# Performance work log

Measured on AMD Instinct MI355X. Metric: run time of the kernel, lower is better.

Reference implementation:

```python
import jax, jax.numpy as jnp
import numpy as np
from jax import lax

T, B, S, H, A = 512, 1024, 64, 128, 10


def setup_inputs() -> dict:
    key = jax.random.key(0)
    ks = jax.random.split(key, 12)
    p = lambda k, shape: jax.random.normal(k, shape, dtype=jnp.float32) * 0.1
    return {
        "x": jax.random.normal(ks[0], (T, B, S), dtype=jnp.float32),
        "W_ih1": p(ks[1], (4 * H, S)),
        "W_hh1": p(ks[2], (4 * H, H)),
        "b_ih1": p(ks[3], (4 * H,)),
        "b_hh1": p(ks[4], (4 * H,)),
        "W_ih2": p(ks[5], (4 * H, H)),
        "W_hh2": p(ks[6], (4 * H, H)),
        "b_ih2": p(ks[7], (4 * H,)),
        "b_hh2": p(ks[8], (4 * H,)),
        "W_out": p(ks[9], (A, H)),
        "b_out": p(ks[10], (A,)),
    }


def _lstm_cell(x_t, h, c, W_ih, W_hh, b_ih, b_hh):
    # PyTorch LSTMCell: gates ordered (i, f, g, o)
    gates = x_t @ W_ih.T + b_ih + h @ W_hh.T + b_hh  # [B, 4H]
    i, f, g, o = jnp.split(gates, 4, axis=-1)
    i = jax.nn.sigmoid(i)
    f = jax.nn.sigmoid(f)
    g = jnp.tanh(g)
    o = jax.nn.sigmoid(o)
    c_new = f * c + i * g
    h_new = o * jnp.tanh(c_new)
    return h_new, c_new


def reference(x, W_ih1, W_hh1, b_ih1, b_hh1, W_ih2, W_hh2, b_ih2, b_hh2, W_out, b_out):
    batch = x.shape[1]
    hdim = W_hh1.shape[1]

    def step(carry, x_t):
        h1, c1, h2, c2 = carry
        h1, c1 = _lstm_cell(x_t, h1, c1, W_ih1, W_hh1, b_ih1, b_hh1)
        h2, c2 = _lstm_cell(h1, h2, c2, W_ih2, W_hh2, b_ih2, b_hh2)
        return (h1, c1, h2, c2), h2

    z = jnp.zeros((batch, hdim), dtype=x.dtype)
    init = (z, z, z, z)
    _, ys = lax.scan(step, init, x)  # ys: [T, B, H]
    mu = ys @ W_out.T + b_out  # deterministic action
    return mu
```

## Files before the change

### kernel.cpp

```cpp
#include <hip/hip_runtime.h>

#define TT 512
#define NB 1024
#define SS 64
#define HH 128
#define NA 10

typedef short bf16x8 __attribute__((ext_vector_type(8)));
typedef float f32x4 __attribute__((ext_vector_type(4)));
typedef unsigned short u16;
typedef unsigned int u32;

__device__ __forceinline__ u16 f2bf(float f){
  union { float f; u32 u; } v; v.f = f;
  return (u16)((v.u + 0x7FFFu + ((v.u >> 16) & 1u)) >> 16);
}
__device__ __forceinline__ float sigm(float v){
  return __builtin_amdgcn_rcpf(1.f + __builtin_amdgcn_exp2f(-1.442695040888963f * v));
}
__device__ __forceinline__ float tanh_(float v){
  return 1.f - 2.f * __builtin_amdgcn_rcpf(1.f + __builtin_amdgcn_exp2f(2.885390081777927f * v));
}
__device__ __forceinline__ void bar_lds(){
  asm volatile("s_waitcnt lgkmcnt(0)" ::: "memory");
  __builtin_amdgcn_s_barrier();
}

__global__ __launch_bounds__(512, 2)
void lstm_fused(const float* __restrict__ x,
                const float* __restrict__ Whh1f,
                const float* __restrict__ bih1, const float* __restrict__ bhh1,
                const float* __restrict__ Wih1f,
                const float* __restrict__ Wih2f,
                const float* __restrict__ Whh2f,
                const float* __restrict__ bih2, const float* __restrict__ bhh2,
                const float* __restrict__ Woutf, const float* __restrict__ boutf,
                float* __restrict__ out)
{
  __shared__ __align__(16) u16 lds[77824];
  u16* whh1s = lds;
  u16* wos   = lds + 65536;
  u16* h1s   = lds + 67584;
  u16* h2s   = lds + 71680;
  u16* xs    = lds + 75776;

  const int tid = threadIdx.x;
  const int w   = tid >> 6;
  const int L   = tid & 63;
  const int Llo = L & 15;
  const int Lhi = L >> 4;
  const int batch0 = blockIdx.x * 16;

#pragma unroll 4
  for (int it = 0; it < 16; ++it){
    int j = it*512 + tid;
    int l = j & 63, g = (j >> 6) & 3, kt = (j >> 8) & 3, ww = (j >> 10) & 7;
    int col = 128*g + 16*ww + (l & 15);
    int k   = kt*32 + (l >> 4)*8;
    const float* s = Whh1f + col*HH + k;
    bf16x8 v;
#pragma unroll
    for (int e = 0; e < 8; ++e) v[e] = (short)f2bf(s[e]);
    *reinterpret_cast<bf16x8*>(&whh1s[j*8]) = v;
  }

  bf16x8 Wih1r[2][4];
#pragma unroll
  for (int kt = 0; kt < 2; ++kt)
#pragma unroll
    for (int g = 0; g < 4; ++g){
      int col = 128*g + 16*w + Llo;
      const float* s = Wih1f + col*SS + kt*32 + Lhi*8;
      bf16x8 v;
#pragma unroll
      for (int e = 0; e < 8; ++e) v[e] = (short)f2bf(s[e]);
      Wih1r[kt][g] = v;
    }
  bf16x8 Wih2r[4][4], Whh2r[4][4];
#pragma unroll
  for (int kt = 0; kt < 4; ++kt)
#pragma unroll
    for (int g = 0; g < 4; ++g){
      int col = 128*g + 16*w + Llo;
      const float* p2 = Wih2f + col*HH + kt*32 + Lhi*8;
      const float* p3 = Whh2f + col*HH + kt*32 + Lhi*8;
      bf16x8 v2, v3;
#pragma unroll
      for (int e = 0; e < 8; ++e){ v2[e] = (short)f2bf(p2[e]); v3[e] = (short)f2bf(p3[e]); }
      Wih2r[kt][g] = v2; Whh2r[kt][g] = v3;
    }

  float bias1[4], bias2[4];
#pragma unroll
  for (int g = 0; g < 4; ++g){
    int col = 128*g + 16*w + Llo;
    bias1[g] = bih1[col] + bhh1[col];
    bias2[g] = bih2[col] + bhh2[col];
  }
  const float boutr = (Llo < NA) ? boutf[Llo] : 0.f;

  if (tid < 256){
    int kt = tid >> 6, l = tid & 63, llo = l & 15, lhi = (l >> 4) & 3;
    bf16x8 v;
#pragma unroll
    for (int e = 0; e < 8; ++e) v[e] = 0;
    if (llo < NA){
      const float* s = Woutf + llo*HH + kt*32 + lhi*8;
#pragma unroll
      for (int e = 0; e < 8; ++e) v[e] = (short)f2bf(s[e]);
    }
    *reinterpret_cast<bf16x8*>(&wos[kt*512 + l*8]) = v;
  }

  {
    uint4 z = {0u,0u,0u,0u};
    *reinterpret_cast<uint4*>(h1s + tid*8) = z;
    *reinterpret_cast<uint4*>(h2s + tid*8) = z;
  }

  f32x4 c1 = {0.f,0.f,0.f,0.f}, c2 = {0.f,0.f,0.f,0.f};

  const int afrag = L*8;
  const int hwIdx = (2*w + (Llo >> 3))*128 + Lhi*32 + (Llo & 7);

  const int xrow = tid >> 5;
  const int xj   = (tid & 31)*2;
  const int xsIdx = ((xj >> 3)*16 + xrow)*8 + (xj & 7);

  {
    float2 xv = *reinterpret_cast<const float2*>(x + ((size_t)(batch0 + xrow))*SS + xj);
    *reinterpret_cast<u32*>(&xs[xsIdx]) = (u32)f2bf(xv.x) | ((u32)f2bf(xv.y) << 16);
  }
  float2 xreg = *reinterpret_cast<const float2*>(x + ((size_t)NB + batch0 + xrow)*SS + xj);

  __syncthreads();

  for (int t = 0; t < TT; ++t){
    const u16* h1r = h1s + ((t+1)&1)*2048;
    u16*       h1w = h1s + (t&1)*2048;
    const u16* h2r = h2s + (t&1)*2048;
    u16*       h2w = h2s + ((t+1)&1)*2048;
    const u16* xsr = xs + (t&1)*1024;
    u16*       xsw = xs + ((t+1)&1)*1024;

    bf16x8 h1f0 = *reinterpret_cast<const bf16x8*>(h1r + afrag);
    bf16x8 h1f1 = *reinterpret_cast<const bf16x8*>(h1r + 512 + afrag);
    bf16x8 h1f2 = *reinterpret_cast<const bf16x8*>(h1r + 1024 + afrag);
    bf16x8 h1f3 = *reinterpret_cast<const bf16x8*>(h1r + 1536 + afrag);

    f32x4 acc2[4];
#pragma unroll
    for (int g = 0; g < 4; ++g){
      f32x4 a = (f32x4){bias2[g], bias2[g], bias2[g], bias2[g]};
      a = __builtin_amdgcn_mfma_f32_16x16x32_bf16(h1f0, Wih2r[0][g], a, 0, 0, 0);
      a = __builtin_amdgcn_mfma_f32_16x16x32_bf16(h1f1, Wih2r[1][g], a, 0, 0, 0);
      a = __builtin_amdgcn_mfma_f32_16x16x32_bf16(h1f2, Wih2r[2][g], a, 0, 0, 0);
      a = __builtin_amdgcn_mfma_f32_16x16x32_bf16(h1f3, Wih2r[3][g], a, 0, 0, 0);
      acc2[g] = a;
    }
    {
      bf16x8 hf = *reinterpret_cast<const bf16x8*>(h2r + afrag);
#pragma unroll
      for (int g = 0; g < 4; ++g) acc2[g] = __builtin_amdgcn_mfma_f32_16x16x32_bf16(hf, Whh2r[0][g], acc2[g], 0, 0, 0);
      hf = *reinterpret_cast<const bf16x8*>(h2r + 512 + afrag);
#pragma unroll
      for (int g = 0; g < 4; ++g) acc2[g] = __builtin_amdgcn_mfma_f32_16x16x32_bf16(hf, Whh2r[1][g], acc2[g], 0, 0, 0);
      hf = *reinterpret_cast<const bf16x8*>(h2r + 1024 + afrag);
#pragma unroll
      for (int g = 0; g < 4; ++g) acc2[g] = __builtin_amdgcn_mfma_f32_16x16x32_bf16(hf, Whh2r[2][g], acc2[g], 0, 0, 0);
      hf = *reinterpret_cast<const bf16x8*>(h2r + 1536 + afrag);
#pragma unroll
      for (int g = 0; g < 4; ++g) acc2[g] = __builtin_amdgcn_mfma_f32_16x16x32_bf16(hf, Whh2r[3][g], acc2[g], 0, 0, 0);
    }

    if (t > 0){
#pragma unroll
      for (int r = 0; r < 4; ++r){
        float iv = sigm(acc2[0][r]);
        float fv = sigm(acc2[1][r]);
        float gv = tanh_(acc2[2][r]);
        float ov = sigm(acc2[3][r]);
        float cn = fv*c2[r] + iv*gv;
        c2[r] = cn;
        h2w[hwIdx + r*8] = f2bf(ov * tanh_(cn));
      }
    }

    f32x4 acc1[4];
#pragma unroll
    for (int g = 0; g < 4; ++g) acc1[g] = (f32x4){bias1[g], bias1[g], bias1[g], bias1[g]};
#pragma unroll
    for (int kt = 0; kt < 4; ++kt){
      bf16x8 wh0 = *reinterpret_cast<const bf16x8*>(&whh1s[w*8192 + (kt*4+0)*512 + afrag]);
      bf16x8 wh1 = *reinterpret_cast<const bf16x8*>(&whh1s[w*8192 + (kt*4+1)*512 + afrag]);
      bf16x8 wh2 = *reinterpret_cast<const bf16x8*>(&whh1s[w*8192 + (kt*4+2)*512 + afrag]);
      bf16x8 wh3 = *reinterpret_cast<const bf16x8*>(&whh1s[w*8192 + (kt*4+3)*512 + afrag]);
      bf16x8 hf = (kt==0) ? h1f0 : (kt==1) ? h1f1 : (kt==2) ? h1f2 : h1f3;
      acc1[0] = __builtin_amdgcn_mfma_f32_16x16x32_bf16(hf, wh0, acc1[0], 0, 0, 0);
      acc1[1] = __builtin_amdgcn_mfma_f32_16x16x32_bf16(hf, wh1, acc1[1], 0, 0, 0);
      acc1[2] = __builtin_amdgcn_mfma_f32_16x16x32_bf16(hf, wh2, acc1[2], 0, 0, 0);
      acc1[3] = __builtin_amdgcn_mfma_f32_16x16x32_bf16(hf, wh3, acc1[3], 0, 0, 0);
    }

    if (w == 0 && t >= 2){
      f32x4 pacc = {boutr, boutr, boutr, boutr};
#pragma unroll
      for (int kt = 0; kt < 4; ++kt){
        bf16x8 ha = *reinterpret_cast<const bf16x8*>(h2r + kt*512 + afrag);
        bf16x8 wb = *reinterpret_cast<const bf16x8*>(&wos[kt*512 + afrag]);
        pacc = __builtin_amdgcn_mfma_f32_16x16x32_bf16(ha, wb, pacc, 0, 0, 0);
      }
      if (Llo < NA){
        size_t o = ((size_t)(t-2)*NB + batch0 + Lhi*4)*NA + Llo;
#pragma unroll
        for (int r = 0; r < 4; ++r) out[o + (size_t)r*NA] = pacc[r];
      }
    }

    *reinterpret_cast<u32*>(xsw + xsIdx) = (u32)f2bf(xreg.x) | ((u32)f2bf(xreg.y) << 16);
    if (t + 2 < TT)
      xreg = *reinterpret_cast<const float2*>(x + ((size_t)(t+2)*NB + batch0 + xrow)*SS + xj);

    {
      bf16x8 xf0 = *reinterpret_cast<const bf16x8*>(xsr + afrag);
      bf16x8 xf1 = *reinterpret_cast<const bf16x8*>(xsr + 512 + afrag);
#pragma unroll
      for (int g = 0; g < 4; ++g){
        acc1[g] = __builtin_amdgcn_mfma_f32_16x16x32_bf16(xf0, Wih1r[0][g], acc1[g], 0, 0, 0);
        acc1[g] = __builtin_amdgcn_mfma_f32_16x16x32_bf16(xf1, Wih1r[1][g], acc1[g], 0, 0, 0);
      }
    }
#pragma unroll
    for (int r = 0; r < 4; ++r){
      float iv = sigm(acc1[0][r]);
      float fv = sigm(acc1[1][r]);
      float gv = tanh_(acc1[2][r]);
      float ov = sigm(acc1[3][r]);
      float cn = fv*c1[r] + iv*gv;
      c1[r] = cn;
      h1w[hwIdx + r*8] = f2bf(ov * tanh_(cn));
    }

    bar_lds();
  }

  {
    const u16* h1r = h1s + ((TT+1)&1)*2048;
    const u16* h2r = h2s + (TT&1)*2048;
    u16*       h2w = h2s + ((TT+1)&1)*2048;

    bf16x8 h1f0 = *reinterpret_cast<const bf16x8*>(h1r + afrag);
    bf16x8 h1f1 = *reinterpret_cast<const bf16x8*>(h1r + 512 + afrag);
    bf16x8 h1f2 = *reinterpret_cast<const bf16x8*>(h1r + 1024 + afrag);
    bf16x8 h1f3 = *reinterpret_cast<const bf16x8*>(h1r + 1536 + afrag);
    bf16x8 h2f0 = *reinterpret_cast<const bf16x8*>(h2r + afrag);
    bf16x8 h2f1 = *reinterpret_cast<const bf16x8*>(h2r + 512 + afrag);
    bf16x8 h2f2 = *reinterpret_cast<const bf16x8*>(h2r + 1024 + afrag);
    bf16x8 h2f3 = *reinterpret_cast<const bf16x8*>(h2r + 1536 + afrag);

    f32x4 acc2[4];
#pragma unroll
    for (int g = 0; g < 4; ++g){
      f32x4 a = (f32x4){bias2[g], bias2[g], bias2[g], bias2[g]};
      a = __builtin_amdgcn_mfma_f32_16x16x32_bf16(h1f0, Wih2r[0][g], a, 0, 0, 0);
      a = __builtin_amdgcn_mfma_f32_16x16x32_bf16(h1f1, Wih2r[1][g], a, 0, 0, 0);
      a = __builtin_amdgcn_mfma_f32_16x16x32_bf16(h1f2, Wih2r[2][g], a, 0, 0, 0);
      a = __builtin_amdgcn_mfma_f32_16x16x32_bf16(h1f3, Wih2r[3][g], a, 0, 0, 0);
      a = __builtin_amdgcn_mfma_f32_16x16x32_bf16(h2f0, Whh2r[0][g], a, 0, 0, 0);
      a = __builtin_amdgcn_mfma_f32_16x16x32_bf16(h2f1, Whh2r[1][g], a, 0, 0, 0);
      a = __builtin_amdgcn_mfma_f32_16x16x32_bf16(h2f2, Whh2r[2][g], a, 0, 0, 0);
      a = __builtin_amdgcn_mfma_f32_16x16x32_bf16(h2f3, Whh2r[3][g], a, 0, 0, 0);
      acc2[g] = a;
    }
#pragma unroll
    for (int r = 0; r < 4; ++r){
      float iv = sigm(acc2[0][r]);
      float fv = sigm(acc2[1][r]);
      float gv = tanh_(acc2[2][r]);
      float ov = sigm(acc2[3][r]);
      float cn = fv*c2[r] + iv*gv;
      c2[r] = cn;
      h2w[hwIdx + r*8] = f2bf(ov * tanh_(cn));
    }

    if (w == 0){
      f32x4 pacc = {boutr, boutr, boutr, boutr};
      pacc = __builtin_amdgcn_mfma_f32_16x16x32_bf16(h2f0, *reinterpret_cast<const bf16x8*>(&wos[afrag]),        pacc, 0, 0, 0);
      pacc = __builtin_amdgcn_mfma_f32_16x16x32_bf16(h2f1, *reinterpret_cast<const bf16x8*>(&wos[512 + afrag]),  pacc, 0, 0, 0);
      pacc = __builtin_amdgcn_mfma_f32_16x16x32_bf16(h2f2, *reinterpret_cast<const bf16x8*>(&wos[1024 + afrag]), pacc, 0, 0, 0);
      pacc = __builtin_amdgcn_mfma_f32_16x16x32_bf16(h2f3, *reinterpret_cast<const bf16x8*>(&wos[1536 + afrag]), pacc, 0, 0, 0);
      if (Llo < NA){
        size_t o = ((size_t)(TT-2)*NB + batch0 + Lhi*4)*NA + Llo;
#pragma unroll
        for (int r = 0; r < 4; ++r) out[o + (size_t)r*NA] = pacc[r];
      }
    }

    bar_lds();

    if (w == 0){
      const u16* h2f = h2s + ((TT+1)&1)*2048;
      bf16x8 a0 = *reinterpret_cast<const bf16x8*>(h2f + afrag);
      bf16x8 a1 = *reinterpret_cast<const bf16x8*>(h2f + 512 + afrag);
      bf16x8 a2 = *reinterpret_cast<const bf16x8*>(h2f + 1024 + afrag);
      bf16x8 a3 = *reinterpret_cast<const bf16x8*>(h2f + 1536 + afrag);
      f32x4 pacc = {boutr, boutr, boutr, boutr};
      pacc = __builtin_amdgcn_mfma_f32_16x16x32_bf16(a0, *reinterpret_cast<const bf16x8*>(&wos[afrag]),        pacc, 0, 0, 0);
      pacc = __builtin_amdgcn_mfma_f32_16x16x32_bf16(a1, *reinterpret_cast<const bf16x8*>(&wos[512 + afrag]),  pacc, 0, 0, 0);
      pacc = __builtin_amdgcn_mfma_f32_16x16x32_bf16(a2, *reinterpret_cast<const bf16x8*>(&wos[1024 + afrag]), pacc, 0, 0, 0);
      pacc = __builtin_amdgcn_mfma_f32_16x16x32_bf16(a3, *reinterpret_cast<const bf16x8*>(&wos[1536 + afrag]), pacc, 0, 0, 0);
      if (Llo < NA){
        size_t o = ((size_t)(TT-1)*NB + batch0 + Lhi*4)*NA + Llo;
#pragma unroll
        for (int r = 0; r < 4; ++r) out[o + (size_t)r*NA] = pacc[r];
      }
    }
  }
}

extern "C" void kernel_launch(void* const* d_in, const int* in_sizes, int n_in,
                              void* d_out, int out_size, void* d_ws, size_t ws_size,
                              hipStream_t stream){
  (void)in_sizes; (void)n_in; (void)out_size; (void)d_ws; (void)ws_size;
  const float* xp   = (const float*)d_in[0];
  const float* wih1 = (const float*)d_in[1];
  const float* whh1 = (const float*)d_in[2];
  const float* bih1 = (const float*)d_in[3];
  const float* bhh1 = (const float*)d_in[4];
  const float* wih2 = (const float*)d_in[5];
  const float* whh2 = (const float*)d_in[6];
  const float* bih2 = (const float*)d_in[7];
  const float* bhh2 = (const float*)d_in[8];
  const float* wout = (const float*)d_in[9];
  const float* bout = (const float*)d_in[10];
  float* outp = (float*)d_out;

  hipLaunchKernelGGL(lstm_fused, dim3(64), dim3(512), 0, stream,
                     xp, whh1, bih1, bhh1, wih1, wih2, whh2, bih2, bhh2, wout, bout,
                     outp);
}
```

Before: 1.451 ms.

## Specialize warps: half compute layer-1 cell, half layer-2 cell

```diff
diff --git a/kernel.cpp b/kernel.cpp
--- a/kernel.cpp
+++ b/kernel.cpp
@@ -38,7 +38,7 @@
                 float* __restrict__ out)
 {
   __shared__ __align__(16) u16 lds[77824];
-  u16* whh1s = lds;
+  u16* whh2s = lds;
   u16* wos   = lds + 65536;
   u16* h1s   = lds + 67584;
   u16* h2s   = lds + 71680;
@@ -50,54 +50,20 @@
   const int Llo = L & 15;
   const int Lhi = L >> 4;
   const int batch0 = blockIdx.x * 16;
+  const int afrag = L*8;
 
 #pragma unroll 4
   for (int it = 0; it < 16; ++it){
     int j = it*512 + tid;
-    int l = j & 63, g = (j >> 6) & 3, kt = (j >> 8) & 3, ww = (j >> 10) & 7;
-    int col = 128*g + 16*ww + (l & 15);
+    int l = j & 63, g = (j >> 6) & 3, kt = (j >> 8) & 3, ss = (j >> 10) & 7;
+    int col = 128*g + 16*ss + (l & 15);
     int k   = kt*32 + (l >> 4)*8;
-    const float* s = Whh1f + col*HH + k;
+    const float* s = Whh2f + col*HH + k;
     bf16x8 v;
 #pragma unroll
     for (int e = 0; e < 8; ++e) v[e] = (short)f2bf(s[e]);
-    *reinterpret_cast<bf16x8*>(&whh1s[j*8]) = v;
-  }
-
-  bf16x8 Wih1r[2][4];
-#pragma unroll
-  for (int kt = 0; kt < 2; ++kt)
-#pragma unroll
-    for (int g = 0; g < 4; ++g){
-      int col = 128*g + 16*w + Llo;
-      const float* s = Wih1f + col*SS + kt*32 + Lhi*8;
-      bf16x8 v;
-#pragma unroll
-      for (int e = 0; e < 8; ++e) v[e] = (short)f2bf(s[e]);
-      Wih1r[kt][g] = v;
-    }
-  bf16x8 Wih2r[4][4], Whh2r[4][4];
-#pragma unroll
-  for (int kt = 0; kt < 4; ++kt)
-#pragma unroll
-    for (int g = 0; g < 4; ++g){
-      int col = 128*g + 16*w + Llo;
-      const float* p2 = Wih2f + col*HH + kt*32 + Lhi*8;
-      const float* p3 = Whh2f + col*HH + kt*32 + Lhi*8;
-      bf16x8 v2, v3;
-#pragma unroll
-      for (int e = 0; e < 8; ++e){ v2[e] = (short)f2bf(p2[e]); v3[e] = (short)f2bf(p3[e]); }
-      Wih2r[kt][g] = v2; Whh2r[kt][g] = v3;
-    }
-
-  float bias1[4], bias2[4];
-#pragma unroll
-  for (int g = 0; g < 4; ++g){
-    int col = 128*g + 16*w + Llo;
-    bias1[g] = bih1[col] + bhh1[col];
-    bias2[g] = bih2[col] + bhh2[col];
-  }
-  const float boutr = (Llo < NA) ? boutf[Llo] : 0.f;
+    *reinterpret_cast<bf16x8*>(&whh2s[j*8]) = v;
+  }
 
   if (tid < 256){
     int kt = tid >> 6, l = tid & 63, llo = l & 15, lhi = (l >> 4) & 3;
@@ -118,20 +84,79 @@
     *reinterpret_cast<uint4*>(h2s + tid*8) = z;
   }
 
-  f32x4 c1 = {0.f,0.f,0.f,0.f}, c2 = {0.f,0.f,0.f,0.f};
-
-  const int afrag = L*8;
-  const int hwIdx = (2*w + (Llo >> 3))*128 + Lhi*32 + (Llo & 7);
-
-  const int xrow = tid >> 5;
-  const int xj   = (tid & 31)*2;
-  const int xsIdx = ((xj >> 3)*16 + xrow)*8 + (xj & 7);
-
-  {
-    float2 xv = *reinterpret_cast<const float2*>(x + ((size_t)(batch0 + xrow))*SS + xj);
-    *reinterpret_cast<u32*>(&xs[xsIdx]) = (u32)f2bf(xv.x) | ((u32)f2bf(xv.y) << 16);
-  }
-  float2 xreg = *reinterpret_cast<const float2*>(x + ((size_t)NB + batch0 + xrow)*SS + xj);
+  const float boutr = (Llo < NA) ? boutf[Llo] : 0.f;
+
+  bf16x8 Wr[2][6][4];
+  float  biasr[2][4];
+  f32x4  cr[2];
+  float4 xreg;
+
+  if (w < 4){
+#pragma unroll
+    for (int si = 0; si < 2; ++si){
+      int s = w + si*4;
+#pragma unroll
+      for (int kt = 0; kt < 4; ++kt)
+#pragma unroll
+        for (int g = 0; g < 4; ++g){
+          int col = 128*g + 16*s + Llo;
+          const float* p = Whh1f + col*HH + kt*32 + Lhi*8;
+          bf16x8 v;
+#pragma unroll
+          for (int e = 0; e < 8; ++e) v[e] = (short)f2bf(p[e]);
+          Wr[si][kt][g] = v;
+        }
+#pragma unroll
+      for (int kt = 0; kt < 2; ++kt)
+#pragma unroll
+        for (int g = 0; g < 4; ++g){
+          int col = 128*g + 16*s + Llo;
+          const float* p = Wih1f + col*SS + kt*32 + Lhi*8;
+          bf16x8 v;
+#pragma unroll
+          for (int e = 0; e < 8; ++e) v[e] = (short)f2bf(p[e]);
+          Wr[si][4+kt][g] = v;
+        }
+#pragma unroll
+      for (int g = 0; g < 4; ++g){
+        int col = 128*g + 16*s + Llo;
+        biasr[si][g] = bih1[col] + bhh1[col];
+      }
+    }
+    {
+      int row = tid & 15, j = (tid >> 4) * 4;
+      int xsIdx = ((j >> 3)*16 + row)*8 + (j & 7);
+      float4 xv = *reinterpret_cast<const float4*>(x + ((size_t)(batch0 + row))*SS + j);
+      u32 lo = (u32)f2bf(xv.x) | ((u32)f2bf(xv.y) << 16);
+      u32 hi = (u32)f2bf(xv.z) | ((u32)f2bf(xv.w) << 16);
+      *reinterpret_cast<uint2*>(xs + xsIdx) = make_uint2(lo, hi);
+      xreg = *reinterpret_cast<const float4*>(x + ((size_t)NB + batch0 + row)*SS + j);
+    }
+  } else {
+#pragma unroll
+    for (int si = 0; si < 2; ++si){
+      int s = (w - 4) + si*4;
+#pragma unroll
+      for (int kt = 0; kt < 4; ++kt)
+#pragma unroll
+        for (int g = 0; g < 4; ++g){
+          int col = 128*g + 16*s + Llo;
+          const float* p = Wih2f + col*HH + kt*32 + Lhi*8;
+          bf16x8 v;
+#pragma unroll
+          for (int e = 0; e < 8; ++e) v[e] = (short)f2bf(p[e]);
+          Wr[si][kt][g] = v;
+        }
+#pragma unroll
+      for (int g = 0; g < 4; ++g){
+        int col = 128*g + 16*s + Llo;
+        biasr[si][g] = bih2[col] + bhh2[col];
+      }
+    }
+  }
+
+#pragma unroll
+  for (int si = 0; si < 2; ++si) cr[si] = (f32x4){0.f,0.f,0.f,0.f};
 
   __syncthreads();
 
@@ -143,66 +168,150 @@
     const u16* xsr = xs + (t&1)*1024;
     u16*       xsw = xs + ((t+1)&1)*1024;
 
-    bf16x8 h1f0 = *reinterpret_cast<const bf16x8*>(h1r + afrag);
-    bf16x8 h1f1 = *reinterpret_cast<const bf16x8*>(h1r + 512 + afrag);
-    bf16x8 h1f2 = *reinterpret_cast<const bf16x8*>(h1r + 1024 + afrag);
-    bf16x8 h1f3 = *reinterpret_cast<const bf16x8*>(h1r + 1536 + afrag);
-
-    f32x4 acc2[4];
-#pragma unroll
-    for (int g = 0; g < 4; ++g){
-      f32x4 a = (f32x4){bias2[g], bias2[g], bias2[g], bias2[g]};
-      a = __builtin_amdgcn_mfma_f32_16x16x32_bf16(h1f0, Wih2r[0][g], a, 0, 0, 0);
-      a = __builtin_amdgcn_mfma_f32_16x16x32_bf16(h1f1, Wih2r[1][g], a, 0, 0, 0);
-      a = __builtin_amdgcn_mfma_f32_16x16x32_bf16(h1f2, Wih2r[2][g], a, 0, 0, 0);
-      a = __builtin_amdgcn_mfma_f32_16x16x32_bf16(h1f3, Wih2r[3][g], a, 0, 0, 0);
-      acc2[g] = a;
-    }
-    {
-      bf16x8 hf = *reinterpret_cast<const bf16x8*>(h2r + afrag);
-#pragma unroll
-      for (int g = 0; g < 4; ++g) acc2[g] = __builtin_amdgcn_mfma_f32_16x16x32_bf16(hf, Whh2r[0][g], acc2[g], 0, 0, 0);
-      hf = *reinterpret_cast<const bf16x8*>(h2r + 512 + afrag);
-#pragma unroll
-      for (int g = 0; g < 4; ++g) acc2[g] = __builtin_amdgcn_mfma_f32_16x16x32_bf16(hf, Whh2r[1][g], acc2[g], 0, 0, 0);
-      hf = *reinterpret_cast<const bf16x8*>(h2r + 1024 + afrag);
-#pragma unroll
-      for (int g = 0; g < 4; ++g) acc2[g] = __builtin_amdgcn_mfma_f32_16x16x32_bf16(hf, Whh2r[2][g], acc2[g], 0, 0, 0);
-      hf = *reinterpret_cast<const bf16x8*>(h2r + 1536 + afrag);
-#pragma unroll
-      for (int g = 0; g < 4; ++g) acc2[g] = __builtin_amdgcn_mfma_f32_16x16x32_bf16(hf, Whh2r[3][g], acc2[g], 0, 0, 0);
-    }
-
-    if (t > 0){
+    if (w < 4){
+      {
+        int row = tid & 15, j = (tid >> 4) * 4;
+        int xsIdx = ((j >> 3)*16 + row)*8 + (j & 7);
+        u32 lo = (u32)f2bf(xreg.x) | ((u32)f2bf(xreg.y) << 16);
+        u32 hi = (u32)f2bf(xreg.z) | ((u32)f2bf(xreg.w) << 16);
+        *reinterpret_cast<uint2*>(xsw + xsIdx) = make_uint2(lo, hi);
+        if (t + 2 < TT)
+          xreg = *reinterpret_cast<const float4*>(x + ((size_t)(t+2)*NB + batch0 + row)*SS + j);
+      }
+#pragma unroll
+      for (int si = 0; si < 2; ++si){
+        int s = w + si*4;
+        f32x4 a0 = (f32x4){biasr[si][0],biasr[si][0],biasr[si][0],biasr[si][0]};
+        f32x4 a1 = (f32x4){biasr[si][1],biasr[si][1],biasr[si][1],biasr[si][1]};
+        f32x4 a2 = (f32x4){biasr[si][2],biasr[si][2],biasr[si][2],biasr[si][2]};
+        f32x4 a3 = (f32x4){biasr[si][3],biasr[si][3],biasr[si][3],biasr[si][3]};
+#pragma unroll
+        for (int kt = 0; kt < 4; ++kt){
+          bf16x8 hf = *reinterpret_cast<const bf16x8*>(h1r + kt*512 + afrag);
+          a0 = __builtin_amdgcn_mfma_f32_16x16x32_bf16(hf, Wr[si][kt][0], a0, 0, 0, 0);
+          a1 = __builtin_amdgcn_mfma_f32_16x16x32_bf16(hf, Wr[si][kt][1], a1, 0, 0, 0);
+          a2 = __builtin_amdgcn_mfma_f32_16x16x32_bf16(hf, Wr[si][kt][2], a2, 0, 0, 0);
+          a3 = __builtin_amdgcn_mfma_f32_16x16x32_bf16(hf, Wr[si][kt][3], a3, 0, 0, 0);
+        }
+#pragma unroll
+        for (int kt = 0; kt < 2; ++kt){
+          bf16x8 xf = *reinterpret_cast<const bf16x8*>(xsr + kt*512 + afrag);
+          a0 = __builtin_amdgcn_mfma_f32_16x16x32_bf16(xf, Wr[si][4+kt][0], a0, 0, 0, 0);
+          a1 = __builtin_amdgcn_mfma_f32_16x16x32_bf16(xf, Wr[si][4+kt][1], a1, 0, 0, 0);
+          a2 = __builtin_amdgcn_mfma_f32_16x16x32_bf16(xf, Wr[si][4+kt][2], a2, 0, 0, 0);
+          a3 = __builtin_amdgcn_mfma_f32_16x16x32_bf16(xf, Wr[si][4+kt][3], a3, 0, 0, 0);
+        }
+        int hwIdx = (2*s + (Llo >> 3))*128 + Lhi*32 + (Llo & 7);
+#pragma unroll
+        for (int r = 0; r < 4; ++r){
+          float iv = sigm(a0[r]);
+          float fv = sigm(a1[r]);
+          float gv = tanh_(a2[r]);
+          float ov = sigm(a3[r]);
+          float cn = fv*cr[si][r] + iv*gv;
+          cr[si][r] = cn;
+          h1w[hwIdx + r*8] = f2bf(ov * tanh_(cn));
+        }
+      }
+    } else {
+#pragma unroll
+      for (int si = 0; si < 2; ++si){
+        int s = (w - 4) + si*4;
+        f32x4 a0 = (f32x4){biasr[si][0],biasr[si][0],biasr[si][0],biasr[si][0]};
+        f32x4 a1 = (f32x4){biasr[si][1],biasr[si][1],biasr[si][1],biasr[si][1]};
+        f32x4 a2 = (f32x4){biasr[si][2],biasr[si][2],biasr[si][2],biasr[si][2]};
+        f32x4 a3 = (f32x4){biasr[si][3],biasr[si][3],biasr[si][3],biasr[si][3]};
+#pragma unroll
+        for (int kt = 0; kt < 4; ++kt){
+          bf16x8 hf1 = *reinterpret_cast<const bf16x8*>(h1r + kt*512 + afrag);
+          a0 = __builtin_amdgcn_mfma_f32_16x16x32_bf16(hf1, Wr[si][kt][0], a0, 0, 0, 0);
+          a1 = __builtin_amdgcn_mfma_f32_16x16x32_bf16(hf1, Wr[si][kt][1], a1, 0, 0, 0);
+          a2 = __builtin_amdgcn_mfma_f32_16x16x32_bf16(hf1, Wr[si][kt][2], a2, 0, 0, 0);
+          a3 = __builtin_amdgcn_mfma_f32_16x16x32_bf16(hf1, Wr[si][kt][3], a3, 0, 0, 0);
+          bf16x8 hf2 = *reinterpret_cast<const bf16x8*>(h2r + kt*512 + afrag);
+          bf16x8 wb0 = *reinterpret_cast<const bf16x8*>(&whh2s[s*8192 + (kt*4+0)*512 + afrag]);
+          bf16x8 wb1 = *reinterpret_cast<const bf16x8*>(&whh2s[s*8192 + (kt*4+1)*512 + afrag]);
+          bf16x8 wb2 = *reinterpret_cast<const bf16x8*>(&whh2s[s*8192 + (kt*4+2)*512 + afrag]);
+          bf16x8 wb3 = *reinterpret_cast<const bf16x8*>(&whh2s[s*8192 + (kt*4+3)*512 + afrag]);
+          a0 = __builtin_amdgcn_mfma_f32_16x16x32_bf16(hf2, wb0, a0, 0, 0, 0);
+          a1 = __builtin_amdgcn_mfma_f32_16x16x32_bf16(hf2, wb1, a1, 0, 0, 0);
+          a2 = __builtin_amdgcn_mfma_f32_16x16x32_bf16(hf2, wb2, a2, 0, 0, 0);
+          a3 = __builtin_amdgcn_mfma_f32_16x16x32_bf16(hf2, wb3, a3, 0, 0, 0);
+        }
+        if (t > 0){
+          int hwIdx = (2*s + (Llo >> 3))*128 + Lhi*32 + (Llo & 7);
+#pragma unroll
+          for (int r = 0; r < 4; ++r){
+            float iv = sigm(a0[r]);
+            float fv = sigm(a1[r]);
+            float gv = tanh_(a2[r]);
+            float ov = sigm(a3[r]);
+            float cn = fv*cr[si][r] + iv*gv;
+            cr[si][r] = cn;
+            h2w[hwIdx + r*8] = f2bf(ov * tanh_(cn));
+          }
+        }
+      }
+      if (w == 4 && t >= 2){
+        f32x4 pacc = {boutr, boutr, boutr, boutr};
+#pragma unroll
+        for (int kt = 0; kt < 4; ++kt){
+          bf16x8 ha = *reinterpret_cast<const bf16x8*>(h2r + kt*512 + afrag);
+          bf16x8 wb = *reinterpret_cast<const bf16x8*>(&wos[kt*512 + afrag]);
+          pacc = __builtin_amdgcn_mfma_f32_16x16x32_bf16(ha, wb, pacc, 0, 0, 0);
+        }
+        if (Llo < NA){
+          size_t o = ((size_t)(t-2)*NB + batch0 + Lhi*4)*NA + Llo;
+#pragma unroll
+          for (int r = 0; r < 4; ++r) out[o + (size_t)r*NA] = pacc[r];
+        }
+      }
+    }
+
+    bar_lds();
+  }
+
+  if (w >= 4){
+    const u16* h1r = h1s + ((TT+1)&1)*2048;
+    const u16* h2r = h2s + (TT&1)*2048;
+    u16*       h2w = h2s + ((TT+1)&1)*2048;
+#pragma unroll
+    for (int si = 0; si < 2; ++si){
+      int s = (w - 4) + si*4;
+      f32x4 a0 = (f32x4){biasr[si][0],biasr[si][0],biasr[si][0],biasr[si][0]};
+      f32x4 a1 = (f32x4){biasr[si][1],biasr[si][1],biasr[si][1],biasr[si][1]};
+      f32x4 a2 = (f32x4){biasr[si][2],biasr[si][2],biasr[si][2],biasr[si][2]};
+      f32x4 a3 = (f32x4){biasr[si][3],biasr[si][3],biasr[si][3],biasr[si][3]};
+#pragma unroll
+      for (int kt = 0; kt < 4; ++kt){
+        bf16x8 hf1 = *reinterpret_cast<const bf16x8*>(h1r + kt*512 + afrag);
+        a0 = __builtin_amdgcn_mfma_f32_16x16x32_bf16(hf1, Wr[si][kt][0], a0, 0, 0, 0);
+        a1 = __builtin_amdgcn_mfma_f32_16x16x32_bf16(hf1, Wr[si][kt][1], a1, 0, 0, 0);
+        a2 = __builtin_amdgcn_mfma_f32_16x16x32_bf16(hf1, Wr[si][kt][2], a2, 0, 0, 0);
+        a3 = __builtin_amdgcn_mfma_f32_16x16x32_bf16(hf1, Wr[si][kt][3], a3, 0, 0, 0);
+        bf16x8 hf2 = *reinterpret_cast<const bf16x8*>(h2r + kt*512 + afrag);
+        bf16x8 wb0 = *reinterpret_cast<const bf16x8*>(&whh2s[s*8192 + (kt*4+0)*512 + afrag]);
+        bf16x8 wb1 = *reinterpret_cast<const bf16x8*>(&whh2s[s*8192 + (kt*4+1)*512 + afrag]);
+        bf16x8 wb2 = *reinterpret_cast<const bf16x8*>(&whh2s[s*8192 + (kt*4+2)*512 + afrag]);
+        bf16x8 wb3 = *reinterpret_cast<const bf16x8*>(&whh2s[s*8192 + (kt*4+3)*512 + afrag]);
+        a0 = __builtin_amdgcn_mfma_f32_16x16x32_bf16(hf2, wb0, a0, 0, 0, 0);
+        a1 = __builtin_amdgcn_mfma_f32_16x16x32_bf16(hf2, wb1, a1, 0, 0, 0);
+        a2 = __builtin_amdgcn_mfma_f32_16x16x32_bf16(hf2, wb2, a2, 0, 0, 0);
+        a3 = __builtin_amdgcn_mfma_f32_16x16x32_bf16(hf2, wb3, a3, 0, 0, 0);
+      }
+      int hwIdx = (2*s + (Llo >> 3))*128 + Lhi*32 + (Llo & 7);
 #pragma unroll
       for (int r = 0; r < 4; ++r){
-        float iv = sigm(acc2[0][r]);
-        float fv = sigm(acc2[1][r]);
-        float gv = tanh_(acc2[2][r]);
-        float ov = sigm(acc2[3][r]);
-        float cn = fv*c2[r] + iv*gv;
-        c2[r] = cn;
+        float iv = sigm(a0[r]);
+        float fv = sigm(a1[r]);
+        float gv = tanh_(a2[r]);
+        float ov = sigm(a3[r]);
+        float cn = fv*cr[si][r] + iv*gv;
+        cr[si][r] = cn;
         h2w[hwIdx + r*8] = f2bf(ov * tanh_(cn));
       }
     }
-
-    f32x4 acc1[4];
-#pragma unroll
-    for (int g = 0; g < 4; ++g) acc1[g] = (f32x4){bias1[g], bias1[g], bias1[g], bias1[g]};
-#pragma unroll
-    for (int kt = 0; kt < 4; ++kt){
-      bf16x8 wh0 = *reinterpret_cast<const bf16x8*>(&whh1s[w*8192 + (kt*4+0)*512 + afrag]);
-      bf16x8 wh1 = *reinterpret_cast<const bf16x8*>(&whh1s[w*8192 + (kt*4+1)*512 + afrag]);
-      bf16x8 wh2 = *reinterpret_cast<const bf16x8*>(&whh1s[w*8192 + (kt*4+2)*512 + afrag]);
-      bf16x8 wh3 = *reinterpret_cast<const bf16x8*>(&whh1s[w*8192 + (kt*4+3)*512 + afrag]);
-      bf16x8 hf = (kt==0) ? h1f0 : (kt==1) ? h1f1 : (kt==2) ? h1f2 : h1f3;
-      acc1[0] = __builtin_amdgcn_mfma_f32_16x16x32_bf16(hf, wh0, acc1[0], 0, 0, 0);
-      acc1[1] = __builtin_amdgcn_mfma_f32_16x16x32_bf16(hf, wh1, acc1[1], 0, 0, 0);
-      acc1[2] = __builtin_amdgcn_mfma_f32_16x16x32_bf16(hf, wh2, acc1[2], 0, 0, 0);
-      acc1[3] = __builtin_amdgcn_mfma_f32_16x16x32_bf16(hf, wh3, acc1[3], 0, 0, 0);
-    }
-
-    if (w == 0 && t >= 2){
+    if (w == 4){
       f32x4 pacc = {boutr, boutr, boutr, boutr};
 #pragma unroll
       for (int kt = 0; kt < 4; ++kt){
@@ -211,109 +320,28 @@
         pacc = __builtin_amdgcn_mfma_f32_16x16x32_bf16(ha, wb, pacc, 0, 0, 0);
       }
       if (Llo < NA){
-        size_t o = ((size_t)(t-2)*NB + batch0 + Lhi*4)*NA + Llo;
+        size_t o = ((size_t)(TT-2)*NB + batch0 + Lhi*4)*NA + Llo;
 #pragma unroll
         for (int r = 0; r < 4; ++r) out[o + (size_t)r*NA] = pacc[r];
       }
     }
-
-    *reinterpret_cast<u32*>(xsw + xsIdx) = (u32)f2bf(xreg.x) | ((u32)f2bf(xreg.y) << 16);
-    if (t + 2 < TT)
-      xreg = *reinterpret_cast<const float2*>(x + ((size_t)(t+2)*NB + batch0 + xrow)*SS + xj);
-
-    {
-      bf16x8 xf0 = *reinterpret_cast<const bf16x8*>(xsr + afrag);
-      bf16x8 xf1 = *reinterpret_cast<const bf16x8*>(xsr + 512 + afrag);
-#pragma unroll
-      for (int g = 0; g < 4; ++g){
-        acc1[g] = __builtin_amdgcn_mfma_f32_16x16x32_bf16(xf0, Wih1r[0][g], acc1[g], 0, 0, 0);
-        acc1[g] = __builtin_amdgcn_mfma_f32_16x16x32_bf16(xf1, Wih1r[1][g], acc1[g], 0, 0, 0);
-      }
-    }
-#pragma unroll
-    for (int r = 0; r < 4; ++r){
-      float iv = sigm(acc1[0][r]);
-      float fv = sigm(acc1[1][r]);
-      float gv = tanh_(acc1[2][r]);
-      float ov = sigm(acc1[3][r]);
-      float cn = fv*c1[r] + iv*gv;
-      c1[r] = cn;
-      h1w[hwIdx + r*8] = f2bf(ov * tanh_(cn));
-    }
-
-    bar_lds();
-  }
-
-  {
-    const u16* h1r = h1s + ((TT+1)&1)*2048;
-    const u16* h2r = h2s + (TT&1)*2048;
-    u16*       h2w = h2s + ((TT+1)&1)*2048;
-
-    bf16x8 h1f0 = *reinterpret_cast<const bf16x8*>(h1r + afrag);
-    bf16x8 h1f1 = *reinterpret_cast<const bf16x8*>(h1r + 512 + afrag);
-    bf16x8 h1f2 = *reinterpret_cast<const bf16x8*>(h1r + 1024 + afrag);
-    bf16x8 h1f3 = *reinterpret_cast<const bf16x8*>(h1r + 1536 + afrag);
-    bf16x8 h2f0 = *reinterpret_cast<const bf16x8*>(h2r + afrag);
-    bf16x8 h2f1 = *reinterpret_cast<const bf16x8*>(h2r + 512 + afrag);
-    bf16x8 h2f2 = *reinterpret_cast<const bf16x8*>(h2r + 1024 + afrag);
-    bf16x8 h2f3 = *reinterpret_cast<const bf16x8*>(h2r + 1536 + afrag);
-
-    f32x4 acc2[4];
-#pragma unroll
-    for (int g = 0; g < 4; ++g){
-      f32x4 a = (f32x4){bias2[g], bias2[g], bias2[g], bias2[g]};
-      a = __builtin_amdgcn_mfma_f32_16x16x32_bf16(h1f0, Wih2r[0][g], a, 0, 0, 0);
-      a = __builtin_amdgcn_mfma_f32_16x16x32_bf16(h1f1, Wih2r[1][g], a, 0, 0, 0);
-      a = __builtin_amdgcn_mfma_f32_16x16x32_bf16(h1f2, Wih2r[2][g], a, 0, 0, 0);
-      a = __builtin_amdgcn_mfma_f32_16x16x32_bf16(h1f3, Wih2r[3][g], a, 0, 0, 0);
-      a = __builtin_amdgcn_mfma_f32_16x16x32_bf16(h2f0, Whh2r[0][g], a, 0, 0, 0);
-      a = __builtin_amdgcn_mfma_f32_16x16x32_bf16(h2f1, Whh2r[1][g], a, 0, 0, 0);
-      a = __builtin_amdgcn_mfma_f32_16x16x32_bf16(h2f2, Whh2r[2][g], a, 0, 0, 0);
-      a = __builtin_amdgcn_mfma_f32_16x16x32_bf16(h2f3, Whh2r[3][g], a, 0, 0, 0);
-      acc2[g] = a;
-    }
-#pragma unroll
-    for (int r = 0; r < 4; ++r){
-      float iv = sigm(acc2[0][r]);
-      float fv = sigm(acc2[1][r]);
-      float gv = tanh_(acc2[2][r]);
-      float ov = sigm(acc2[3][r]);
-      float cn = fv*c2[r] + iv*gv;
-      c2[r] = cn;
-      h2w[hwIdx + r*8] = f2bf(ov * tanh_(cn));
-    }
-
-    if (w == 0){
-      f32x4 pacc = {boutr, boutr, boutr, boutr};
-      pacc = __builtin_amdgcn_mfma_f32_16x16x32_bf16(h2f0, *reinterpret_cast<const bf16x8*>(&wos[afrag]),        pacc, 0, 0, 0);
-      pacc = __builtin_amdgcn_mfma_f32_16x16x32_bf16(h2f1, *reinterpret_cast<const bf16x8*>(&wos[512 + afrag]),  pacc, 0, 0, 0);
-      pacc = __builtin_amdgcn_mfma_f32_16x16x32_bf16(h2f2, *reinterpret_cast<const bf16x8*>(&wos[1024 + afrag]), pacc, 0, 0, 0);
-      pacc = __builtin_amdgcn_mfma_f32_16x16x32_bf16(h2f3, *reinterpret_cast<const bf16x8*>(&wos[1536 + afrag]), pacc, 0, 0, 0);
-      if (Llo < NA){
-        size_t o = ((size_t)(TT-2)*NB + batch0 + Lhi*4)*NA + Llo;
-#pragma unroll
-        for (int r = 0; r < 4; ++r) out[o + (size_t)r*NA] = pacc[r];
-      }
-    }
-
-    bar_lds();
-
-    if (w == 0){
-      const u16* h2f = h2s + ((TT+1)&1)*2048;
-      bf16x8 a0 = *reinterpret_cast<const bf16x8*>(h2f + afrag);
-      bf16x8 a1 = *reinterpret_cast<const bf16x8*>(h2f + 512 + afrag);
-      bf16x8 a2 = *reinterpret_cast<const bf16x8*>(h2f + 1024 + afrag);
-      bf16x8 a3 = *reinterpret_cast<const bf16x8*>(h2f + 1536 + afrag);
-      f32x4 pacc = {boutr, boutr, boutr, boutr};
-      pacc = __builtin_amdgcn_mfma_f32_16x16x32_bf16(a0, *reinterpret_cast<const bf16x8*>(&wos[afrag]),        pacc, 0, 0, 0);
-      pacc = __builtin_amdgcn_mfma_f32_16x16x32_bf16(a1, *reinterpret_cast<const bf16x8*>(&wos[512 + afrag]),  pacc, 0, 0, 0);
-      pacc = __builtin_amdgcn_mfma_f32_16x16x32_bf16(a2, *reinterpret_cast<const bf16x8*>(&wos[1024 + afrag]), pacc, 0, 0, 0);
-      pacc = __builtin_amdgcn_mfma_f32_16x16x32_bf16(a3, *reinterpret_cast<const bf16x8*>(&wos[1536 + afrag]), pacc, 0, 0, 0);
-      if (Llo < NA){
-        size_t o = ((size_t)(TT-1)*NB + batch0 + Lhi*4)*NA + Llo;
-#pragma unroll
-        for (int r = 0; r < 4; ++r) out[o + (size_t)r*NA] = pacc[r];
-      }
+  }
+
+  bar_lds();
+
+  if (w == 4){
+    const u16* h2f = h2s + ((TT+1)&1)*2048;
+    f32x4 pacc = {boutr, boutr, boutr, boutr};
+#pragma unroll
+    for (int kt = 0; kt < 4; ++kt){
+      bf16x8 ha = *reinterpret_cast<const bf16x8*>(h2f + kt*512 + afrag);
+      bf16x8 wb = *reinterpret_cast<const bf16x8*>(&wos[kt*512 + afrag]);
+      pacc = __builtin_amdgcn_mfma_f32_16x16x32_bf16(ha, wb, pacc, 0, 0, 0);
+    }
+    if (Llo < NA){
+      size_t o = ((size_t)(TT-1)*NB + batch0 + Lhi*4)*NA + Llo;
+#pragma unroll
+      for (int r = 0; r < 4; ++r) out[o + (size_t)r*NA] = pacc[r];
     }
   }
 }
```

After: 1.857 ms. 28.0% more time.
